# Optimization experiments

Hardware: AMD Instinct MI355X
Metric: run time of the kernel (lower is better)

The kernel has to match this reference:

```python
import jax, jax.numpy as jnp
import numpy as np

DEPTH = 10
N_FEATURES = 1024
N_INTERNAL = 2 ** DEPTH - 1  # 1023
N_LEAVES = 2 ** DEPTH        # 1024
BATCH = 16384


def setup_inputs() -> dict:
    key = jax.random.key(0)
    k_x, k_w, k_b, k_leaf = jax.random.split(key, 4)
    x = jax.random.normal(k_x, (BATCH, N_FEATURES), dtype=jnp.float32)
    # stacked nn.Linear(n_features, 1) weights for all internal nodes
    bound = 1.0 / np.sqrt(N_FEATURES)
    W = jax.random.uniform(k_w, (N_INTERNAL, N_FEATURES), dtype=jnp.float32, minval=-bound, maxval=bound)
    b = jax.random.uniform(k_b, (N_INTERNAL,), dtype=jnp.float32, minval=-bound, maxval=bound)
    leaf_values = jax.random.normal(k_leaf, (N_LEAVES, 1), dtype=jnp.float32) * 0.01
    return {"x": x, "W": W, "b": b, "leaf_values": leaf_values}


def reference(x, W, b, leaf_values):
    # all node gates in one GEMM: [B, n_internal]
    gates = jax.nn.sigmoid(x @ W.T + b)
    # leaf path bits, MSB-first (matches path[::-1] in the original).
    # NOTE: original code increments node_index 0..depth-1 for every leaf
    # (it does NOT do binary-tree child indexing) -- replicated faithfully.
    leaf_ids = jnp.arange(N_LEAVES)
    shifts = DEPTH - 1 - jnp.arange(DEPTH)
    bits = ((leaf_ids[:, None] >> shifts[None, :]) & 1).astype(bool)  # [L, D]
    prob = jnp.ones((x.shape[0], N_LEAVES), dtype=x.dtype)  # [B, L]
    for d in range(DEPTH):  # small fixed loop over tree depth
        p = gates[:, d:d + 1]  # [B, 1]
        prob = prob * jnp.where(bits[:, d][None, :], p, 1.0 - p)
    return prob @ leaf_values  # [B, 1]
```

## Files before the change

kernel.cpp:

```cpp
#include <hip/hip_runtime.h>

#define BATCH   16384
#define NF      1024
#define NWAVES  2048


template <int CTRL>
__device__ __forceinline__ float dpp_add(float x) {
    int xi = __builtin_bit_cast(int, x);
    int yi = __builtin_amdgcn_update_dpp(xi, xi, CTRL, 0xf, 0xf, false);
    return x + __builtin_bit_cast(float, yi);
}

__device__ __forceinline__ float row_reduce_dpp(float x) {
    x = dpp_add<0xB1>(x);
    x = dpp_add<0x4E>(x);
    x = dpp_add<0x124>(x);
    x = dpp_add<0x128>(x);
    return x;
}

__device__ __forceinline__ float wave_sum(float x) {
    float r = row_reduce_dpp(x);
    int ri = __builtin_bit_cast(int, r);
    float s0 = __builtin_bit_cast(float, __builtin_amdgcn_readlane(ri, 0));
    float s1 = __builtin_bit_cast(float, __builtin_amdgcn_readlane(ri, 16));
    float s2 = __builtin_bit_cast(float, __builtin_amdgcn_readlane(ri, 32));
    float s3 = __builtin_bit_cast(float, __builtin_amdgcn_readlane(ri, 48));
    return (s0 + s1) + (s2 + s3);
}

__global__ __launch_bounds__(256, 2)
void sdt_kernel(const float* __restrict__ x,
                const float* __restrict__ W,
                const float* __restrict__ b,
                const float* __restrict__ leaf,
                float* __restrict__ out)
{
    const int lane = threadIdx.x & 63;
    const int wid  = (int)((blockIdx.x * blockDim.x + threadIdx.x) >> 6);

    float4 Wr[10][4];
#pragma unroll
    for (int d = 0; d < 10; ++d)
#pragma unroll
        for (int k = 0; k < 4; ++k)
            Wr[d][k] = *reinterpret_cast<const float4*>(W + d * NF + k * 256 + 4 * lane);

    float bias[10];
#pragma unroll
    for (int d = 0; d < 10; ++d) bias[d] = b[d];

    float Lv[16];
#pragma unroll
    for (int k = 0; k < 4; ++k) {
        float4 t = *reinterpret_cast<const float4*>(leaf + 16 * lane + 4 * k);
        Lv[4 * k + 0] = t.x; Lv[4 * k + 1] = t.y;
        Lv[4 * k + 2] = t.z; Lv[4 * k + 3] = t.w;
    }

    float4 xv[4];
    {
        const float* xr = x + (size_t)wid * NF;
#pragma unroll
        for (int k = 0; k < 4; ++k)
            xv[k] = *reinterpret_cast<const float4*>(xr + k * 256 + 4 * lane);
    }

    for (int row = wid; row < BATCH; row += NWAVES) {
        float4 xn[4];
        const int nrow = row + NWAVES;
        if (nrow < BATCH) {
            const float* xr = x + (size_t)nrow * NF;
#pragma unroll
            for (int k = 0; k < 4; ++k)
                xn[k] = *reinterpret_cast<const float4*>(xr + k * 256 + 4 * lane);
        }

        float acc[10];
#pragma unroll
        for (int d = 0; d < 10; ++d) {
            float a = 0.0f;
#pragma unroll
            for (int k = 0; k < 4; ++k) {
                a = fmaf(xv[k].x, Wr[d][k].x, a);
                a = fmaf(xv[k].y, Wr[d][k].y, a);
                a = fmaf(xv[k].z, Wr[d][k].z, a);
                a = fmaf(xv[k].w, Wr[d][k].w, a);
            }
            acc[d] = a;
        }

        float g[10], gc[10];
#pragma unroll
        for (int d = 0; d < 10; ++d) {
            float z = wave_sum(acc[d]) + bias[d];
            float e = __expf(-z);
            g[d]  = __builtin_amdgcn_rcpf(1.0f + e);
            gc[d] = e * g[d];
        }

        float s9[8];
#pragma unroll
        for (int j = 0; j < 8; ++j)
            s9[j] = fmaf(g[9], Lv[2 * j + 1] - Lv[2 * j], Lv[2 * j]);
        float s8[4];
#pragma unroll
        for (int j = 0; j < 4; ++j)
            s8[j] = fmaf(g[8], s9[2 * j + 1] - s9[2 * j], s9[2 * j]);
        float s7[2];
#pragma unroll
        for (int j = 0; j < 2; ++j)
            s7[j] = fmaf(g[7], s8[2 * j + 1] - s8[2 * j], s8[2 * j]);
        float s6 = fmaf(g[6], s7[1] - s7[0], s7[0]);

        float w = 1.0f;
#pragma unroll
        for (int d = 0; d < 6; ++d) {
            int bit = (lane >> (5 - d)) & 1;
            w *= bit ? g[d] : gc[d];
        }

        float v = wave_sum(w * s6);
        if (lane == 0) out[row] = v;

#pragma unroll
        for (int k = 0; k < 4; ++k) xv[k] = xn[k];
    }
}

extern "C" void kernel_launch(void* const* d_in, const int* in_sizes, int n_in,
                              void* d_out, int out_size, void* d_ws, size_t ws_size,
                              hipStream_t stream) {
    const float* x    = (const float*)d_in[0];
    const float* W    = (const float*)d_in[1];
    const float* b    = (const float*)d_in[2];
    const float* leaf = (const float*)d_in[3];
    float* out = (float*)d_out;

    const int blocks  = 512;
    const int threads = 256;

    sdt_kernel<<<blocks, threads, 0, stream>>>(x, W, b, leaf, out);
}
```

Measured before the change: 26.12 us.

## Triple-buffer x row prefetch with full unroll and move leaf values to LDS

New measurement: 25.27 us. 1.03x faster.

```diff
diff --git a/kernel.cpp b/kernel.cpp
--- a/kernel.cpp
+++ b/kernel.cpp
@@ -3,6 +3,7 @@
 #define BATCH   16384
 #define NF      1024
 #define NWAVES  2048
+#define NITER   (BATCH / NWAVES)
 
 
 template <int CTRL>
@@ -40,6 +41,16 @@
     const int lane = threadIdx.x & 63;
     const int wid  = (int)((blockIdx.x * blockDim.x + threadIdx.x) >> 6);
 
+    __shared__ float lv_t[1024];
+    {
+        const int t = threadIdx.x * 4;
+#pragma unroll
+        for (int e = 0; e < 4; ++e) {
+            int idx = t + e;
+            lv_t[idx] = leaf[(idx & 63) * 16 + (idx >> 6)];
+        }
+    }
+
     float4 Wr[10][4];
 #pragma unroll
     for (int d = 0; d < 10; ++d)
@@ -51,32 +62,16 @@
 #pragma unroll
     for (int d = 0; d < 10; ++d) bias[d] = b[d];
 
-    float Lv[16];
-#pragma unroll
-    for (int k = 0; k < 4; ++k) {
-        float4 t = *reinterpret_cast<const float4*>(leaf + 16 * lane + 4 * k);
-        Lv[4 * k + 0] = t.x; Lv[4 * k + 1] = t.y;
-        Lv[4 * k + 2] = t.z; Lv[4 * k + 3] = t.w;
-    }
+    __syncthreads();
 
-    float4 xv[4];
-    {
-        const float* xr = x + (size_t)wid * NF;
+    auto load_row = [&](float4 (&dst)[4], int r) {
+        const float* xr = x + (size_t)r * NF;
 #pragma unroll
         for (int k = 0; k < 4; ++k)
-            xv[k] = *reinterpret_cast<const float4*>(xr + k * 256 + 4 * lane);
-    }
+            dst[k] = *reinterpret_cast<const float4*>(xr + k * 256 + 4 * lane);
+    };
 
-    for (int row = wid; row < BATCH; row += NWAVES) {
-        float4 xn[4];
-        const int nrow = row + NWAVES;
-        if (nrow < BATCH) {
-            const float* xr = x + (size_t)nrow * NF;
-#pragma unroll
-            for (int k = 0; k < 4; ++k)
-                xn[k] = *reinterpret_cast<const float4*>(xr + k * 256 + 4 * lane);
-        }
-
+    auto process_row = [&](const float4 (&xv)[4], int row) {
         float acc[10];
 #pragma unroll
         for (int d = 0; d < 10; ++d) {
@@ -90,20 +85,19 @@
             }
             acc[d] = a;
         }
-
-        float g[10], gc[10];
+        float g[10];
 #pragma unroll
         for (int d = 0; d < 10; ++d) {
             float z = wave_sum(acc[d]) + bias[d];
-            float e = __expf(-z);
-            g[d]  = __builtin_amdgcn_rcpf(1.0f + e);
-            gc[d] = e * g[d];
+            g[d] = __builtin_amdgcn_rcpf(1.0f + __expf(-z));
         }
-
         float s9[8];
 #pragma unroll
-        for (int j = 0; j < 8; ++j)
-            s9[j] = fmaf(g[9], Lv[2 * j + 1] - Lv[2 * j], Lv[2 * j]);
+        for (int j = 0; j < 8; ++j) {
+            float La = lv_t[(2 * j) * 64 + lane];
+            float Lb = lv_t[(2 * j + 1) * 64 + lane];
+            s9[j] = fmaf(g[9], Lb - La, La);
+        }
         float s8[4];
 #pragma unroll
         for (int j = 0; j < 4; ++j)
@@ -118,15 +112,25 @@
 #pragma unroll
         for (int d = 0; d < 6; ++d) {
             int bit = (lane >> (5 - d)) & 1;
-            w *= bit ? g[d] : gc[d];
+            w *= bit ? g[d] : (1.0f - g[d]);
         }
 
         float v = wave_sum(w * s6);
         if (lane == 0) out[row] = v;
+    };
 
-#pragma unroll
-        for (int k = 0; k < 4; ++k) xv[k] = xn[k];
-    }
+    float4 xb0[4], xb1[4], xb2[4];
+    load_row(xb0, wid);
+    load_row(xb1, wid + 1 * NWAVES);
+
+    load_row(xb2, wid + 2 * NWAVES); process_row(xb0, wid);
+    load_row(xb0, wid + 3 * NWAVES); process_row(xb1, wid + 1 * NWAVES);
+    load_row(xb1, wid + 4 * NWAVES); process_row(xb2, wid + 2 * NWAVES);
+    load_row(xb2, wid + 5 * NWAVES); process_row(xb0, wid + 3 * NWAVES);
+    load_row(xb0, wid + 6 * NWAVES); process_row(xb1, wid + 4 * NWAVES);
+    load_row(xb1, wid + 7 * NWAVES); process_row(xb2, wid + 5 * NWAVES);
+    process_row(xb0, wid + 6 * NWAVES);
+    process_row(xb1, wid + 7 * NWAVES);
 }
 
 extern "C" void kernel_launch(void* const* d_in, const int* in_sizes, int n_in,
```
